# Performance work log

Measured on AMD Instinct MI355X. Metric: run time of the kernel, lower is better.

The kernel has to match this reference:

```python
import jax, jax.numpy as jnp
import numpy as np

HIDDEN = 1024
NUM_HEADS = 16
GROUP_SIZE = 2
GROUP_NUM = NUM_HEADS // GROUP_SIZE
HEAD_DIM = HIDDEN // NUM_HEADS


def setup_inputs() -> dict:
    key = jax.random.key(0)
    ks = jax.random.split(key, 9)
    B, S = 1, 4096
    s = 0.02
    return {
        "hidden_state": jax.random.normal(ks[0], (B, S, HIDDEN), jnp.float32),
        "Wq": jax.random.normal(ks[1], (HIDDEN, HIDDEN), jnp.float32) * s,
        "bq": jnp.zeros((HIDDEN,), jnp.float32),
        "Wk": jax.random.normal(ks[2], (HIDDEN, GROUP_NUM * HEAD_DIM), jnp.float32) * s,
        "bk": jnp.zeros((GROUP_NUM * HEAD_DIM,), jnp.float32),
        "Wv": jax.random.normal(ks[3], (HIDDEN, GROUP_NUM * HEAD_DIM), jnp.float32) * s,
        "bv": jnp.zeros((GROUP_NUM * HEAD_DIM,), jnp.float32),
        "Wo": jax.random.normal(ks[4], (HIDDEN, HIDDEN), jnp.float32) * s,
        "bo": jnp.zeros((HIDDEN,), jnp.float32),
    }


def reference(hidden_state, Wq, bq, Wk, bk, Wv, bv, Wo, bo):
    B, S, _ = hidden_state.shape
    # projections
    q = hidden_state @ Wq + bq                      # [B,S,H*hd]
    k = hidden_state @ Wk + bk                      # [B,S,G*hd]
    v = hidden_state @ Wv + bv                      # [B,S,G*hd]
    q = q.reshape(B, S, NUM_HEADS, HEAD_DIM).transpose(0, 2, 1, 3)   # [B,H,S,hd]
    k = k.reshape(B, S, GROUP_NUM, HEAD_DIM).transpose(0, 2, 1, 3)   # [B,G,S,hd]
    v = v.reshape(B, S, GROUP_NUM, HEAD_DIM).transpose(0, 2, 1, 3)
    # expand KV heads: each kv head repeated group_size times consecutively
    k = jnp.repeat(k, GROUP_SIZE, axis=1)           # [B,H,S,hd]
    v = jnp.repeat(v, GROUP_SIZE, axis=1)
    scale = 1.0 / np.sqrt(HEAD_DIM).astype(np.float32)
    scores = jnp.einsum('bhqd,bhkd->bhqk', q, k) * scale   # [B,H,S,S]
    attn = jax.nn.softmax(scores, axis=-1)
    ctx = jnp.einsum('bhqk,bhkd->bhqd', attn, v)    # [B,H,S,hd]
    ctx = ctx.transpose(0, 2, 1, 3).reshape(B, S, HIDDEN)
    return ctx @ Wo + bo
```

## Files before the change

kernel.cpp:

```cpp
#include <hip/hip_runtime.h>
#include <hip/hip_bf16.h>
#include <cstdint>
#include <cstddef>

typedef __bf16 bf16x8 __attribute__((ext_vector_type(8)));
typedef float f32x4 __attribute__((ext_vector_type(4)));
typedef float f32x16 __attribute__((ext_vector_type(16)));
typedef uint32_t u32x4 __attribute__((ext_vector_type(4)));
typedef __hip_bfloat16 bf16h;

__device__ __forceinline__ unsigned short bf16bits(float f) {
  bf16h h = __float2bfloat16(f);
  return __builtin_bit_cast(unsigned short, h);
}

__global__ void cast_f32_bf16(const float* __restrict__ src, bf16h* __restrict__ dst, int n) {
  int i = (blockIdx.x * blockDim.x + threadIdx.x) * 4;
  if (i >= n) return;
  float4 v = *reinterpret_cast<const float4*>(src + i);
  ushort4 o;
  o.x = bf16bits(v.x); o.y = bf16bits(v.y); o.z = bf16bits(v.z); o.w = bf16bits(v.w);
  *reinterpret_cast<ushort4*>(dst + i) = o;
}

__global__ __launch_bounds__(256) void prep_weights(const float* __restrict__ Wq, const float* __restrict__ Wk,
                                                    const float* __restrict__ Wv, const float* __restrict__ Wo,
                                                    const float* __restrict__ bq, const float* __restrict__ bk,
                                                    const float* __restrict__ bv,
                                                    bf16h* __restrict__ WcT, bf16h* __restrict__ WoT,
                                                    float* __restrict__ bcat, float qscale) {
  int b = blockIdx.x;
  int tx = threadIdx.x, ty = threadIdx.y;
  if (b >= 3072) {
    int i = (b - 3072) * 256 + ty * 32 + tx;
    bcat[i] = (i < 1024) ? bq[i] * qscale : (i < 1536 ? bk[i - 1024] : bv[i - 1536]);
    return;
  }
  const float* src; bf16h* dst; int C, bx, by; float sc = 1.0f;
  if (b < 1024)      { src = Wq; dst = WcT;               C = 1024; bx = b & 31;          by = b >> 5; sc = qscale; }
  else if (b < 1536) { src = Wk; dst = WcT + 1024 * 1024; C = 512;  bx = (b - 1024) & 15; by = (b - 1024) >> 4; }
  else if (b < 2048) { src = Wv; dst = WcT + 1536 * 1024; C = 512;  bx = (b - 1536) & 15; by = (b - 1536) >> 4; }
  else               { src = Wo; dst = WoT;               C = 1024; bx = (b - 2048) & 31; by = (b - 2048) >> 5; }
  __shared__ float tile[32][33];
  int c0 = bx * 32, r0 = by * 32;
  #pragma unroll
  for (int i = 0; i < 32; i += 8)
    tile[ty + i][tx] = src[(size_t)(r0 + ty + i) * C + c0 + tx];
  __syncthreads();
  #pragma unroll
  for (int i = 0; i < 32; i += 8)
    dst[(size_t)(c0 + ty + i) * 1024 + r0 + tx] = __float2bfloat16(tile[tx][ty + i] * sc);
}

__global__ __launch_bounds__(256) void gemm_qkv(const bf16h* __restrict__ A, const bf16h* __restrict__ BT,
                                                const float* __restrict__ bias,
                                                bf16h* __restrict__ qb, bf16h* __restrict__ kperm,
                                                bf16h* __restrict__ vperm) {
  __shared__ __align__(16) bf16h As[128 * 64];
  __shared__ __align__(16) bf16h Bs[128 * 64];
  const int tid = threadIdx.x;
  const int lane = tid & 63;
  const int m0 = blockIdx.y * 128, n0 = blockIdx.x * 128;
  const int wid = tid >> 6, wr = wid >> 1, wc = wid & 1;
  const int cl = lane & 15, rg = lane >> 4;
  const int srow = tid >> 3, scol = (tid & 7) * 8;
  const int K = 1024;
  f32x4 acc[4][4] = {};

  for (int k0 = 0; k0 < K; k0 += 64) {
    __syncthreads();
    #pragma unroll
    for (int i = 0; i < 4; ++i) {
      int r = i * 32 + srow;
      __builtin_amdgcn_global_load_lds(
          (__attribute__((address_space(1))) void*)(A + (size_t)(m0 + r) * K + k0 + scol),
          (__attribute__((address_space(3))) void*)(As + i * 2048 + tid * 8), 16, 0, 0);
    }
    #pragma unroll
    for (int i = 0; i < 4; ++i) {
      int r = i * 32 + srow;
      __builtin_amdgcn_global_load_lds(
          (__attribute__((address_space(1))) void*)(BT + (size_t)(n0 + r) * K + k0 + scol),
          (__attribute__((address_space(3))) void*)(Bs + i * 2048 + tid * 8), 16, 0, 0);
    }
    __syncthreads();
    #pragma unroll
    for (int ks = 0; ks < 2; ++ks) {
      bf16x8 af[4], bfr[4];
      #pragma unroll
      for (int mi = 0; mi < 4; ++mi)
        af[mi] = *reinterpret_cast<const bf16x8*>(As + (wr * 64 + mi * 16 + cl) * 64 + ks * 32 + rg * 8);
      #pragma unroll
      for (int ni = 0; ni < 4; ++ni)
        bfr[ni] = *reinterpret_cast<const bf16x8*>(Bs + (wc * 64 + ni * 16 + cl) * 64 + ks * 32 + rg * 8);
      #pragma unroll
      for (int mi = 0; mi < 4; ++mi)
        #pragma unroll
        for (int ni = 0; ni < 4; ++ni)
          acc[mi][ni] = __builtin_amdgcn_mfma_f32_16x16x32_bf16(af[mi], bfr[ni], acc[mi][ni], 0, 0, 0);
    }
  }

  if (n0 < 1024) {
    #pragma unroll
    for (int ni = 0; ni < 4; ++ni) {
      int col = n0 + wc * 64 + ni * 16 + cl;
      float bv = bias[col];
      #pragma unroll
      for (int mi = 0; mi < 4; ++mi)
        #pragma unroll
        for (int j = 0; j < 4; ++j) {
          int row = m0 + wr * 64 + mi * 16 + rg * 4 + j;
          qb[(size_t)row * 1024 + col] = __float2bfloat16(acc[mi][ni][j] + bv);
        }
    }
  } else if (n0 < 1536) {
    #pragma unroll
    for (int ni = 0; ni < 4; ++ni) {
      int col = n0 + wc * 64 + ni * 16 + cl;
      float bv = bias[col];
      int cd = col - 1024, gg = cd >> 6, d = cd & 63;
      int ds = d >> 4, hh = (d >> 3) & 1, e = d & 7;
      size_t cbase = (size_t)gg * 262144 + (size_t)ds * 512 + hh * 256 + e;
      #pragma unroll
      for (int mi = 0; mi < 4; ++mi) {
        int row0 = m0 + wr * 64 + mi * 16 + rg * 4;
        #pragma unroll
        for (int j = 0; j < 4; ++j) {
          int k = row0 + j;
          kperm[cbase + (size_t)(k >> 5) * 2048 + (k & 31) * 8] = __float2bfloat16(acc[mi][ni][j] + bv);
        }
      }
    }
  } else {
    #pragma unroll
    for (int ni = 0; ni < 4; ++ni) {
      int col = n0 + wc * 64 + ni * 16 + cl;
      float bv = bias[col];
      int cd = col - 1536, gg = cd >> 6, d = cd & 63;
      int l31 = d & 31, dh = d >> 5;
      #pragma unroll
      for (int mi = 0; mi < 4; ++mi) {
        int row0 = m0 + wr * 64 + mi * 16 + rg * 4;
        int kt = row0 >> 5, ks = (row0 >> 4) & 1, hh = (row0 >> 3) & 1, e0 = row0 & 7;
        ushort4 o;
        o.x = bf16bits(acc[mi][ni][0] + bv);
        o.y = bf16bits(acc[mi][ni][1] + bv);
        o.z = bf16bits(acc[mi][ni][2] + bv);
        o.w = bf16bits(acc[mi][ni][3] + bv);
        *reinterpret_cast<ushort4*>(vperm + ((size_t)gg * 128 + kt) * 2048 +
                                    (size_t)(ks * 2 + dh) * 512 + (hh * 32 + l31) * 8 + e0) = o;
      }
    }
  }
}

__global__ __launch_bounds__(256) void gemm_bt(const bf16h* __restrict__ A, const bf16h* __restrict__ BT,
                                               const float* __restrict__ bias, float* __restrict__ C,
                                               int M, int N, int K) {
  __shared__ __align__(16) bf16h As[128 * 64];
  __shared__ __align__(16) bf16h Bs[128 * 64];
  const int tid = threadIdx.x;
  const int lane = tid & 63;
  const int m0 = blockIdx.y * 128, n0 = blockIdx.x * 128;
  const int wid = tid >> 6, wr = wid >> 1, wc = wid & 1;
  const int cl = lane & 15, rg = lane >> 4;
  const int srow = tid >> 3, scol = (tid & 7) * 8;
  f32x4 acc[4][4] = {};

  for (int k0 = 0; k0 < K; k0 += 64) {
    __syncthreads();
    #pragma unroll
    for (int i = 0; i < 4; ++i) {
      int r = i * 32 + srow;
      __builtin_amdgcn_global_load_lds(
          (__attribute__((address_space(1))) void*)(A + (size_t)(m0 + r) * K + k0 + scol),
          (__attribute__((address_space(3))) void*)(As + i * 2048 + tid * 8), 16, 0, 0);
    }
    #pragma unroll
    for (int i = 0; i < 4; ++i) {
      int r = i * 32 + srow;
      __builtin_amdgcn_global_load_lds(
          (__attribute__((address_space(1))) void*)(BT + (size_t)(n0 + r) * K + k0 + scol),
          (__attribute__((address_space(3))) void*)(Bs + i * 2048 + tid * 8), 16, 0, 0);
    }
    __syncthreads();
    #pragma unroll
    for (int ks = 0; ks < 2; ++ks) {
      bf16x8 af[4], bfr[4];
      #pragma unroll
      for (int mi = 0; mi < 4; ++mi)
        af[mi] = *reinterpret_cast<const bf16x8*>(As + (wr * 64 + mi * 16 + cl) * 64 + ks * 32 + rg * 8);
      #pragma unroll
      for (int ni = 0; ni < 4; ++ni)
        bfr[ni] = *reinterpret_cast<const bf16x8*>(Bs + (wc * 64 + ni * 16 + cl) * 64 + ks * 32 + rg * 8);
      #pragma unroll
      for (int mi = 0; mi < 4; ++mi)
        #pragma unroll
        for (int ni = 0; ni < 4; ++ni)
          acc[mi][ni] = __builtin_amdgcn_mfma_f32_16x16x32_bf16(af[mi], bfr[ni], acc[mi][ni], 0, 0, 0);
    }
  }
  #pragma unroll
  for (int ni = 0; ni < 4; ++ni) {
    int col = n0 + wc * 64 + ni * 16 + cl;
    float bv = bias[col];
    #pragma unroll
    for (int mi = 0; mi < 4; ++mi)
      #pragma unroll
      for (int j = 0; j < 4; ++j) {
        int row = m0 + wr * 64 + mi * 16 + rg * 4 + j;
        C[(size_t)row * N + col] = acc[mi][ni][j] + bv;
      }
  }
}

__global__ __launch_bounds__(256, 2) void attn_fwd(const bf16h* __restrict__ qb,
                                                   const bf16h* __restrict__ kperm,
                                                   const bf16h* __restrict__ vperm,
                                                   bf16h* __restrict__ ctx) {
  __shared__ float oL[4][64][33];
  __shared__ float lsL[4][64];
  const int t256 = threadIdx.x;
  const int wid = t256 >> 6, lane = t256 & 63;
  const int l31 = lane & 31, hi = lane >> 5;
  const int bid = blockIdx.x;
  const int g = bid & 7, hl = (bid >> 3) & 1, qx = bid >> 4;
  const int h = g * 2 + hl;
  const int q0 = qx * 64;
  const int kt0 = wid * 32;

  bf16x8 qfA[4], qfB[4];
  {
    const bf16h* qrA = qb + (size_t)(q0 + l31) * 1024 + h * 64 + hi * 8;
    #pragma unroll
    for (int ds = 0; ds < 4; ++ds) {
      qfA[ds] = *reinterpret_cast<const bf16x8*>(qrA + ds * 16);
      qfB[ds] = *reinterpret_cast<const bf16x8*>(qrA + (size_t)32 * 1024 + ds * 16);
    }
  }

  const bf16h* kg = kperm + ((size_t)g << 18) + lane * 8;
  const bf16h* vg = vperm + ((size_t)g << 18) + lane * 8;

  f32x16 oA0, oA1, oB0, oB1;
  #pragma unroll
  for (int i = 0; i < 16; ++i) { oA0[i] = 0.f; oA1[i] = 0.f; oB0[i] = 0.f; oB1[i] = 0.f; }
  float lsA = 0.f, lsB = 0.f;

  auto LOAD = [&](bf16x8 (&Kf)[4], bf16x8 (&Vf)[4], int kt) {
    const bf16h* kb = kg + (size_t)kt * 2048;
    const bf16h* vb = vg + (size_t)kt * 2048;
    #pragma unroll
    for (int s = 0; s < 4; ++s) {
      Kf[s] = *reinterpret_cast<const bf16x8*>(kb + s * 512);
      Vf[s] = *reinterpret_cast<const bf16x8*>(vb + s * 512);
    }
  };

  auto build_pa = [&](const f32x16& S, int u) -> bf16x8 {
    uint32_t w0, w1, w2, w3;
    asm("v_cvt_pk_bf16_f32 %0, %1, %2" : "=v"(w0) : "v"(S[8 * u + 0]), "v"(S[8 * u + 1]));
    asm("v_cvt_pk_bf16_f32 %0, %1, %2" : "=v"(w1) : "v"(S[8 * u + 2]), "v"(S[8 * u + 3]));
    asm("v_cvt_pk_bf16_f32 %0, %1, %2" : "=v"(w2) : "v"(S[8 * u + 4]), "v"(S[8 * u + 5]));
    asm("v_cvt_pk_bf16_f32 %0, %1, %2" : "=v"(w3) : "v"(S[8 * u + 6]), "v"(S[8 * u + 7]));
    asm("v_permlane32_swap_b32 %0, %1" : "+v"(w0), "+v"(w2));
    asm("v_permlane32_swap_b32 %0, %1" : "+v"(w1), "+v"(w3));
    u32x4 pw; pw[0] = w0; pw[1] = w1; pw[2] = w2; pw[3] = w3;
    return __builtin_bit_cast(bf16x8, pw);
  };

  auto BODY = [&](const bf16x8 (&Kf)[4], const bf16x8 (&Vf)[4]) {
    f32x16 sA, sB;
    #pragma unroll
    for (int i = 0; i < 16; ++i) { sA[i] = 0.f; sB[i] = 0.f; }
    __builtin_amdgcn_s_setprio(1);
    #pragma unroll
    for (int ds = 0; ds < 4; ++ds) {
      sA = __builtin_amdgcn_mfma_f32_32x32x16_bf16(Kf[ds], qfA[ds], sA, 0, 0, 0);
      sB = __builtin_amdgcn_mfma_f32_32x32x16_bf16(Kf[ds], qfB[ds], sB, 0, 0, 0);
    }
    __builtin_amdgcn_s_setprio(0);
    float ra0 = 0.f, ra1 = 0.f, rb0 = 0.f, rb1 = 0.f;
    #pragma unroll
    for (int r = 0; r < 16; r += 4) {
      #pragma unroll
      for (int j = 0; j < 4; ++j) {
        sA[r + j] = __builtin_amdgcn_exp2f(sA[r + j]);
        sB[r + j] = __builtin_amdgcn_exp2f(sB[r + j]);
      }
      ra0 += sA[r] + sA[r + 1]; ra1 += sA[r + 2] + sA[r + 3];
      rb0 += sB[r] + sB[r + 1]; rb1 += sB[r + 2] + sB[r + 3];
    }
    float rsA = ra0 + ra1, rsB = rb0 + rb1;
    lsA += rsA + __shfl_xor(rsA, 32);
    lsB += rsB + __shfl_xor(rsB, 32);
    __builtin_amdgcn_s_setprio(1);
    #pragma unroll
    for (int u = 0; u < 2; ++u) {
      bf16x8 paA = build_pa(sA, u);
      bf16x8 paB = build_pa(sB, u);
      oA0 = __builtin_amdgcn_mfma_f32_32x32x16_bf16(Vf[u * 2 + 0], paA, oA0, 0, 0, 0);
      oA1 = __builtin_amdgcn_mfma_f32_32x32x16_bf16(Vf[u * 2 + 1], paA, oA1, 0, 0, 0);
      oB0 = __builtin_amdgcn_mfma_f32_32x32x16_bf16(Vf[u * 2 + 0], paB, oB0, 0, 0, 0);
      oB1 = __builtin_amdgcn_mfma_f32_32x32x16_bf16(Vf[u * 2 + 1], paB, oB1, 0, 0, 0);
    }
    __builtin_amdgcn_s_setprio(0);
  };

  bf16x8 Ka[4], Va[4], Kb[4], Vb[4];
  LOAD(Ka, Va, kt0);
  for (int tt = 0; tt < 32; tt += 2) {
    LOAD(Kb, Vb, kt0 + tt + 1);
    BODY(Ka, Va);
    int t2 = (tt + 2 <= 31) ? kt0 + tt + 2 : kt0 + 31;
    LOAD(Ka, Va, t2);
    BODY(Kb, Vb);
  }

  auto merge_pass = [&](const f32x16& x0, const f32x16& x1, float lsv, int qbase) {
    #pragma unroll
    for (int i = 0; i < 16; ++i) {
      oL[wid][lane][i] = x0[i];
      oL[wid][lane][16 + i] = x1[i];
    }
    lsL[wid][lane] = lsv;
    __syncthreads();
    float inv = 1.0f / (lsL[0][lane] + lsL[1][lane] + lsL[2][lane] + lsL[3][lane]);
    const int r0 = 8 * wid;
    float m[8];
    #pragma unroll
    for (int k = 0; k < 8; ++k)
      m[k] = (oL[0][lane][r0 + k] + oL[1][lane][r0 + k] +
              oL[2][lane][r0 + k] + oL[3][lane][r0 + k]) * inv;
    bf16h* op = ctx + (size_t)(qbase + l31) * 1024 + h * 64;
    #pragma unroll
    for (int half = 0; half < 2; ++half) {
      int r = r0 + half * 4;
      int d0 = 32 * (r >> 4) + 8 * ((r & 15) >> 2) + 4 * hi;
      ushort4 st;
      st.x = bf16bits(m[half * 4 + 0]); st.y = bf16bits(m[half * 4 + 1]);
      st.z = bf16bits(m[half * 4 + 2]); st.w = bf16bits(m[half * 4 + 3]);
      *reinterpret_cast<ushort4*>(op + d0) = st;
    }
    __syncthreads();
  };
  merge_pass(oA0, oA1, lsA, q0);
  merge_pass(oB0, oB1, lsB, q0 + 32);
}

extern "C" void kernel_launch(void* const* d_in, const int* in_sizes, int n_in,
                              void* d_out, int out_size, void* d_ws, size_t ws_size,
                              hipStream_t stream) {
  const float* hs = (const float*)d_in[0];
  const float* Wq = (const float*)d_in[1];
  const float* bq = (const float*)d_in[2];
  const float* Wk = (const float*)d_in[3];
  const float* bk = (const float*)d_in[4];
  const float* Wv = (const float*)d_in[5];
  const float* bv = (const float*)d_in[6];
  const float* Wo = (const float*)d_in[7];
  const float* bo = (const float*)d_in[8];
  float* out = (float*)d_out;

  const float QSCALE = 0.125f * 1.44269504088896f;

  char* ws = (char*)d_ws;
  const size_t MB = 1u << 20;
  bf16h* hb    = (bf16h*)(ws);
  bf16h* ctx   = (bf16h*)(ws);
  bf16h* WcT   = (bf16h*)(ws + 8 * MB);
  bf16h* qb    = (bf16h*)(ws + 12 * MB);
  bf16h* kperm = (bf16h*)(ws + 20 * MB);
  bf16h* vperm = (bf16h*)(ws + 24 * MB);
  bf16h* WoT   = (bf16h*)(ws + 28 * MB);
  float* bcat  = (float*)(ws + 30 * MB);

  cast_f32_bf16<<<dim3(4096), dim3(256), 0, stream>>>(hs, hb, 4096 * 1024);
  prep_weights<<<dim3(3080), dim3(32, 8), 0, stream>>>(Wq, Wk, Wv, Wo, bq, bk, bv,
                                                       WcT, WoT, bcat, QSCALE);
  gemm_qkv<<<dim3(16, 32), dim3(256), 0, stream>>>(hb, WcT, bcat, qb, kperm, vperm);
  attn_fwd<<<dim3(1024), dim3(256), 0, stream>>>(qb, kperm, vperm, ctx);
  gemm_bt<<<dim3(8, 32), dim3(256), 0, stream>>>(ctx, WoT, bo, out, 4096, 1024, 1024);
}
```

Before: 144.7 us.

## Merge prep kernels, halve output GEMM tile width, defer row-sum shuffle

Merges the activation cast and weight prep into a single launch to drop one kernel launch. Narrows the output projection GEMM tile from 128 to 64 columns, doubling the grid from 256 to 512 blocks so it fills more CUs, at the cost of re-reading the A tile more often. In attention, the cross-half shuffle of the softmax row sum moves out of the inner loop and is done once after the loop.

```diff
diff --git a/kernel.cpp b/kernel.cpp
--- a/kernel.cpp
+++ b/kernel.cpp
@@ -14,28 +14,30 @@
   return __builtin_bit_cast(unsigned short, h);
 }
 
-__global__ void cast_f32_bf16(const float* __restrict__ src, bf16h* __restrict__ dst, int n) {
-  int i = (blockIdx.x * blockDim.x + threadIdx.x) * 4;
-  if (i >= n) return;
-  float4 v = *reinterpret_cast<const float4*>(src + i);
-  ushort4 o;
-  o.x = bf16bits(v.x); o.y = bf16bits(v.y); o.z = bf16bits(v.z); o.w = bf16bits(v.w);
-  *reinterpret_cast<ushort4*>(dst + i) = o;
-}
-
-__global__ __launch_bounds__(256) void prep_weights(const float* __restrict__ Wq, const float* __restrict__ Wk,
-                                                    const float* __restrict__ Wv, const float* __restrict__ Wo,
-                                                    const float* __restrict__ bq, const float* __restrict__ bk,
-                                                    const float* __restrict__ bv,
-                                                    bf16h* __restrict__ WcT, bf16h* __restrict__ WoT,
-                                                    float* __restrict__ bcat, float qscale) {
+__global__ __launch_bounds__(256) void prep_all(const float* __restrict__ hs, bf16h* __restrict__ hb,
+                                                const float* __restrict__ Wq, const float* __restrict__ Wk,
+                                                const float* __restrict__ Wv, const float* __restrict__ Wo,
+                                                const float* __restrict__ bq, const float* __restrict__ bk,
+                                                const float* __restrict__ bv,
+                                                bf16h* __restrict__ WcT, bf16h* __restrict__ WoT,
+                                                float* __restrict__ bcat, float qscale) {
   int b = blockIdx.x;
-  int tx = threadIdx.x, ty = threadIdx.y;
+  int tid = threadIdx.x;
+  if (b < 4096) {
+    int i = (b * 256 + tid) * 4;
+    float4 v = *reinterpret_cast<const float4*>(hs + i);
+    ushort4 o;
+    o.x = bf16bits(v.x); o.y = bf16bits(v.y); o.z = bf16bits(v.z); o.w = bf16bits(v.w);
+    *reinterpret_cast<ushort4*>(hb + i) = o;
+    return;
+  }
+  b -= 4096;
   if (b >= 3072) {
-    int i = (b - 3072) * 256 + ty * 32 + tx;
+    int i = (b - 3072) * 256 + tid;
     bcat[i] = (i < 1024) ? bq[i] * qscale : (i < 1536 ? bk[i - 1024] : bv[i - 1536]);
     return;
   }
+  int tx = tid & 31, ty = tid >> 5;
   const float* src; bf16h* dst; int C, bx, by; float sc = 1.0f;
   if (b < 1024)      { src = Wq; dst = WcT;               C = 1024; bx = b & 31;          by = b >> 5; sc = qscale; }
   else if (b < 1536) { src = Wk; dst = WcT + 1024 * 1024; C = 512;  bx = (b - 1024) & 15; by = (b - 1024) >> 4; }
@@ -159,14 +161,14 @@
                                                const float* __restrict__ bias, float* __restrict__ C,
                                                int M, int N, int K) {
   __shared__ __align__(16) bf16h As[128 * 64];
-  __shared__ __align__(16) bf16h Bs[128 * 64];
+  __shared__ __align__(16) bf16h Bs[64 * 64];
   const int tid = threadIdx.x;
   const int lane = tid & 63;
-  const int m0 = blockIdx.y * 128, n0 = blockIdx.x * 128;
+  const int m0 = blockIdx.y * 128, n0 = blockIdx.x * 64;
   const int wid = tid >> 6, wr = wid >> 1, wc = wid & 1;
   const int cl = lane & 15, rg = lane >> 4;
   const int srow = tid >> 3, scol = (tid & 7) * 8;
-  f32x4 acc[4][4] = {};
+  f32x4 acc[4][2] = {};
 
   for (int k0 = 0; k0 < K; k0 += 64) {
     __syncthreads();
@@ -178,32 +180,33 @@
           (__attribute__((address_space(3))) void*)(As + i * 2048 + tid * 8), 16, 0, 0);
     }
     #pragma unroll
-    for (int i = 0; i < 4; ++i) {
-      int r = i * 32 + srow;
+    for (int i = 0; i < 2; ++i) {
+      int s = tid + i * 256;
+      int r = s >> 3, c = (s & 7) * 8;
       __builtin_amdgcn_global_load_lds(
-          (__attribute__((address_space(1))) void*)(BT + (size_t)(n0 + r) * K + k0 + scol),
-          (__attribute__((address_space(3))) void*)(Bs + i * 2048 + tid * 8), 16, 0, 0);
+          (__attribute__((address_space(1))) void*)(BT + (size_t)(n0 + r) * K + k0 + c),
+          (__attribute__((address_space(3))) void*)(Bs + s * 8), 16, 0, 0);
     }
     __syncthreads();
     #pragma unroll
     for (int ks = 0; ks < 2; ++ks) {
-      bf16x8 af[4], bfr[4];
+      bf16x8 af[4], bfr[2];
       #pragma unroll
       for (int mi = 0; mi < 4; ++mi)
         af[mi] = *reinterpret_cast<const bf16x8*>(As + (wr * 64 + mi * 16 + cl) * 64 + ks * 32 + rg * 8);
       #pragma unroll
-      for (int ni = 0; ni < 4; ++ni)
-        bfr[ni] = *reinterpret_cast<const bf16x8*>(Bs + (wc * 64 + ni * 16 + cl) * 64 + ks * 32 + rg * 8);
+      for (int ni = 0; ni < 2; ++ni)
+        bfr[ni] = *reinterpret_cast<const bf16x8*>(Bs + (wc * 32 + ni * 16 + cl) * 64 + ks * 32 + rg * 8);
       #pragma unroll
       for (int mi = 0; mi < 4; ++mi)
         #pragma unroll
-        for (int ni = 0; ni < 4; ++ni)
+        for (int ni = 0; ni < 2; ++ni)
           acc[mi][ni] = __builtin_amdgcn_mfma_f32_16x16x32_bf16(af[mi], bfr[ni], acc[mi][ni], 0, 0, 0);
     }
   }
   #pragma unroll
-  for (int ni = 0; ni < 4; ++ni) {
-    int col = n0 + wc * 64 + ni * 16 + cl;
+  for (int ni = 0; ni < 2; ++ni) {
+    int col = n0 + wc * 32 + ni * 16 + cl;
     float bv = bias[col];
     #pragma unroll
     for (int mi = 0; mi < 4; ++mi)
@@ -292,9 +295,8 @@
       ra0 += sA[r] + sA[r + 1]; ra1 += sA[r + 2] + sA[r + 3];
       rb0 += sB[r] + sB[r + 1]; rb1 += sB[r + 2] + sB[r + 3];
     }
-    float rsA = ra0 + ra1, rsB = rb0 + rb1;
-    lsA += rsA + __shfl_xor(rsA, 32);
-    lsB += rsB + __shfl_xor(rsB, 32);
+    lsA += ra0 + ra1;
+    lsB += rb0 + rb1;
     __builtin_amdgcn_s_setprio(1);
     #pragma unroll
     for (int u = 0; u < 2; ++u) {
@@ -317,6 +319,9 @@
     LOAD(Ka, Va, t2);
     BODY(Kb, Vb);
   }
+
+  lsA += __shfl_xor(lsA, 32);
+  lsB += __shfl_xor(lsB, 32);
 
   auto merge_pass = [&](const f32x16& x0, const f32x16& x1, float lsv, int qbase) {
     #pragma unroll
@@ -376,10 +381,9 @@
   bf16h* WoT   = (bf16h*)(ws + 28 * MB);
   float* bcat  = (float*)(ws + 30 * MB);
 
-  cast_f32_bf16<<<dim3(4096), dim3(256), 0, stream>>>(hs, hb, 4096 * 1024);
-  prep_weights<<<dim3(3080), dim3(32, 8), 0, stream>>>(Wq, Wk, Wv, Wo, bq, bk, bv,
-                                                       WcT, WoT, bcat, QSCALE);
+  prep_all<<<dim3(4096 + 3080), dim3(256), 0, stream>>>(hs, hb, Wq, Wk, Wv, Wo, bq, bk, bv,
+                                                        WcT, WoT, bcat, QSCALE);
   gemm_qkv<<<dim3(16, 32), dim3(256), 0, stream>>>(hb, WcT, bcat, qb, kperm, vperm);
   attn_fwd<<<dim3(1024), dim3(256), 0, stream>>>(qb, kperm, vperm, ctx);
-  gemm_bt<<<dim3(8, 32), dim3(256), 0, stream>>>(ctx, WoT, bo, out, 4096, 1024, 1024);
-}
+  gemm_bt<<<dim3(16, 32), dim3(256), 0, stream>>>(ctx, WoT, bo, out, 4096, 1024, 1024);
+}
```

Result: faster. 133.7 us (-7.6%).
